# Performance work log

Measured on AMD Instinct MI355X. Metric: run time of the kernel, lower is better.

## Reference

```python
import math
import jax, jax.numpy as jnp
import numpy as np

B, NQ, NK, DIM, H, HD = 2, 1024, 2048, 1024, 16, 64


def setup_inputs() -> dict:
    key = jax.random.key(0)
    ks = jax.random.split(key, 12)
    s = 1.0 / math.sqrt(DIM)
    return {
        "q": jax.random.normal(ks[0], (B, NQ, DIM), jnp.float32),
        "k": jax.random.normal(ks[1], (B, NK, DIM), jnp.float32),
        "v": jax.random.normal(ks[2], (B, NK, DIM), jnp.float32),
        "distances": jax.random.uniform(ks[3], (B, NQ, NK), jnp.float32),
        "attn_mask": jax.random.bernoulli(ks[4], 0.5, (B, NQ, NK)),
        "key_padding_mask_q": jax.random.bernoulli(ks[5], 0.5, (B, NQ)),
        "key_padding_mask_k": jax.random.bernoulli(ks[6], 0.5, (B, NK)),
        "Wq": jax.random.normal(ks[7], (H * HD, DIM), jnp.float32) * s,
        "Wk": jax.random.normal(ks[8], (H * HD, DIM), jnp.float32) * s,
        "Wv": jax.random.normal(ks[9], (H * HD, DIM), jnp.float32) * s,
        "Wo": jax.random.normal(ks[10], (DIM, H * HD), jnp.float32) * s,
        "gate_alpha": jnp.float32(0.1),
    }


def reference(q, k, v, distances, attn_mask, key_padding_mask_q,
              key_padding_mask_k, Wq, Wk, Wv, Wo, gate_alpha):
    bsz, q_len, _ = q.shape
    k_len = k.shape[1]
    neg = jnp.finfo(q.dtype).min

    # projections -> (B, H, N, HD)
    qp = (q @ Wq.T).reshape(bsz, q_len, H, HD).transpose(0, 2, 1, 3)
    kp = (k @ Wk.T).reshape(bsz, k_len, H, HD).transpose(0, 2, 1, 3)
    vp = (v @ Wv.T).reshape(bsz, k_len, H, HD).transpose(0, 2, 1, 3)

    scores = jnp.einsum('bhqd,bhkd->bhqk', qp, kp) / math.sqrt(HD)
    scores = jnp.where(attn_mask[:, None, :, :], scores, neg)
    scores = jnp.where(key_padding_mask_k[:, None, None, :], scores, neg)

    attn = jax.nn.softmax(scores, axis=-1)  # (B,H,NQ,NK)

    # distance gating: mask, batch-mean normalize, exponential gate
    d = distances * attn_mask.astype(distances.dtype)
    d = d * key_padding_mask_k[:, None, :].astype(d.dtype)
    mean = d.sum(axis=(-1, -2)) / (q_len * k_len + 1e-6)
    mean = jnp.maximum(mean, 1e-6)[:, None, None]
    d = d / mean
    alpha = jax.nn.softplus(gate_alpha)
    gate = jnp.exp(-alpha * d)[:, None, :, :]  # (B,1,NQ,NK)

    w = attn * gate
    w = w / (w.sum(axis=-1, keepdims=True) + 1e-6)

    out = jnp.einsum('bhqk,bhkd->bhqd', w, vp)
    out = out.transpose(0, 2, 1, 3).reshape(bsz, q_len, H * HD)
    out = out * key_padding_mask_q[:, :, None].astype(out.dtype)
    return out @ Wo.T
```

## Files before the change

kernel.cpp:

```cpp
#include <hip/hip_runtime.h>
#include <hip/hip_bf16.h>
#include <cfloat>

#define B_   2
#define NQ_  1024
#define NK_  2048
#define H_   16
#define HD_  64
#define VPAD 2176
#define GPAD 2112

typedef float  floatx4 __attribute__((ext_vector_type(4)));
typedef __bf16 bf16x8  __attribute__((ext_vector_type(8)));
typedef __bf16 bf16x4  __attribute__((ext_vector_type(4)));

static __device__ __forceinline__ floatx4 mfma16(bf16x8 a, bf16x8 b, floatx4 c) {
    return __builtin_amdgcn_mfma_f32_16x16x32_bf16(a, b, c, 0, 0, 0);
}

static __device__ __forceinline__ void gl_lds(const __bf16* g, __bf16* lbase,
                                              int lane) {
#if __has_builtin(__builtin_amdgcn_global_load_lds)
    __builtin_amdgcn_global_load_lds(
        (const __attribute__((address_space(1))) void*)g,
        (__attribute__((address_space(3))) void*)lbase, 16, 0, 0);
#else
    *(bf16x8*)(lbase + lane * 8) = *(const bf16x8*)g;
#endif
}

struct CvtArgs {
    const float* src[7];
    __bf16*      dst[7];
};

__global__ __launch_bounds__(256) void cvt_mean_kernel(
    CvtArgs a, const float* __restrict__ dist, const int* __restrict__ amask,
    const int* __restrict__ kpmk, float* __restrict__ msum,
    __bf16* __restrict__ dmask)
{
    if (blockIdx.x >= 1792) {
        const int mb = blockIdx.x - 1792;
        const int b  = mb >> 9;
        const float* d  = dist  + (size_t)b * NQ_ * NK_;
        const int*   am = amask + (size_t)b * NQ_ * NK_;
        const int*   km = kpmk  + b * NK_;
        __bf16*      dm = dmask + (size_t)b * NQ_ * GPAD;
        const int base = (mb & 511) * 256 + threadIdx.x;
        float s = 0.f;
        #pragma unroll
        for (int j = 0; j < 4; j++) {
            const int i   = base + j * 131072;
            const int idx = i * 4;
            const int kk  = idx & (NK_ - 1);
            const int q   = i >> 9;
            float4 dv = *(const float4*)(d + idx);
            int4   mv = *(const int4*)(am + idx);
            int4   kv = *(const int4*)(km + kk);
            bf16x4 o;
            if (mv.x && kv.x) { s += dv.x; o[0] = (__bf16)dv.x; } else o[0] = (__bf16)3e38f;
            if (mv.y && kv.y) { s += dv.y; o[1] = (__bf16)dv.y; } else o[1] = (__bf16)3e38f;
            if (mv.z && kv.z) { s += dv.z; o[2] = (__bf16)dv.z; } else o[2] = (__bf16)3e38f;
            if (mv.w && kv.w) { s += dv.w; o[3] = (__bf16)dv.w; } else o[3] = (__bf16)3e38f;
            *(bf16x4*)&dm[(size_t)q * GPAD + kk] = o;
        }
        #pragma unroll
        for (int off = 32; off >= 1; off >>= 1) s += __shfl_down(s, off);
        __shared__ float wsum[4];
        if ((threadIdx.x & 63) == 0) wsum[threadIdx.x >> 6] = s;
        __syncthreads();
        if (threadIdx.x == 0)
            atomicAdd(&msum[b], wsum[0] + wsum[1] + wsum[2] + wsum[3]);
        return;
    }
    #pragma unroll
    for (int j = 0; j < 4; j++) {
        size_t r = (size_t)blockIdx.x * 1024 + j * 256 + threadIdx.x;
        int s;
        if (r < 262144)                  { s = 0; }
        else if ((r -= 262144) < 524288) { s = 1; }
        else if ((r -= 524288) < 524288) { s = 2; }
        else { r -= 524288; s = 3 + (int)(r >> 17); r &= 131071; }
        const float* sp = a.src[s] + r * 8;
        float4 f0 = *(const float4*)sp;
        float4 f1 = *(const float4*)(sp + 4);
        bf16x8 o;
        o[0] = (__bf16)f0.x; o[1] = (__bf16)f0.y; o[2] = (__bf16)f0.z; o[3] = (__bf16)f0.w;
        o[4] = (__bf16)f1.x; o[5] = (__bf16)f1.y; o[6] = (__bf16)f1.z; o[7] = (__bf16)f1.w;
        *(bf16x8*)(a.dst[s] + r * 8) = o;
    }
}

template <typename EPI>
static __device__ __forceinline__ void gemm128_core(
    const __bf16* __restrict__ A, const __bf16* __restrict__ Bw,
    int m0, int n0, __bf16* As, __bf16* Bs, EPI epi)
{
    const int t    = threadIdx.x;
    const int w    = t >> 6, lane = t & 63;
    const int lrow = lane & 15, quad = lane >> 4;
    const int lr   = lane >> 2, lc = lane & 3;

    floatx4 acc[4][4];
    #pragma unroll
    for (int mi = 0; mi < 4; mi++)
        #pragma unroll
        for (int ni = 0; ni < 4; ni++) acc[mi][ni] = floatx4{0.f, 0.f, 0.f, 0.f};

    const __bf16* ga = A  + (size_t)(m0 + w * 32 + lr) * 1024 + lc * 8;
    const __bf16* gb = Bw + (size_t)(n0 + w * 32 + lr) * 1024 + lc * 8;

    for (int k0 = 0; k0 < 1024; k0 += 64) {
        __syncthreads();
        #pragma unroll
        for (int h = 0; h < 2; h++) {
            gl_lds(ga + k0 + h * 32,             &As[h * 4096 + (w * 32) * 32],      lane);
            gl_lds(ga + k0 + h * 32 + 16 * 1024, &As[h * 4096 + (w * 32 + 16) * 32], lane);
            gl_lds(gb + k0 + h * 32,             &Bs[h * 4096 + (w * 32) * 32],      lane);
            gl_lds(gb + k0 + h * 32 + 16 * 1024, &Bs[h * 4096 + (w * 32 + 16) * 32], lane);
        }
        __syncthreads();

        #pragma unroll
        for (int h = 0; h < 2; h++) {
            bf16x8 af[4], bfr[4];
            #pragma unroll
            for (int mi = 0; mi < 4; mi++)
                af[mi] = *(const bf16x8*)
                    &As[h * 4096 + ((w & 1) * 64 + mi * 16 + lrow) * 32 + quad * 8];
            #pragma unroll
            for (int ni = 0; ni < 4; ni++)
                bfr[ni] = *(const bf16x8*)
                    &Bs[h * 4096 + ((w >> 1) * 64 + ni * 16 + lrow) * 32 + quad * 8];
            #pragma unroll
            for (int mi = 0; mi < 4; mi++)
                #pragma unroll
                for (int ni = 0; ni < 4; ni++)
                    acc[mi][ni] = mfma16(af[mi], bfr[ni], acc[mi][ni]);
        }
    }

    #pragma unroll
    for (int mi = 0; mi < 4; mi++)
        #pragma unroll
        for (int ni = 0; ni < 4; ni++)
            #pragma unroll
            for (int r = 0; r < 4; r++) {
                const int m = m0 + (w & 1) * 64 + mi * 16 + quad * 4 + r;
                const int n = n0 + (w >> 1) * 64 + ni * 16 + lrow;
                epi(m, n, acc[mi][ni][r]);
            }
}

template <typename EPI>
static __device__ __forceinline__ void gemm32_core(
    const __bf16* __restrict__ A, const __bf16* __restrict__ Bw,
    int m0, int n0, EPI epi)
{
    __shared__ alignas(16) __bf16 As[2][32 * 32];
    __shared__ alignas(16) __bf16 Bs[2][128 * 32];
    const int t    = threadIdx.x;
    const int w    = t >> 6, lane = t & 63;
    const int lrow = lane & 15, quad = lane >> 4;
    const int lr   = lane >> 2, lc = lane & 3;

    floatx4 acc[2][2];
    #pragma unroll
    for (int mi = 0; mi < 2; mi++)
        #pragma unroll
        for (int ni = 0; ni < 2; ni++) acc[mi][ni] = floatx4{0.f, 0.f, 0.f, 0.f};

    const __bf16* ga = A  + (size_t)(m0 + (w & 1) * 16 + lr) * 1024 + lc * 8;
    const __bf16* gb = Bw + (size_t)(n0 + w * 32 + lr) * 1024 + lc * 8;

    for (int k0 = 0; k0 < 1024; k0 += 64) {
        __syncthreads();
        #pragma unroll
        for (int h = 0; h < 2; h++) {
            if (w < 2)
                gl_lds(ga + k0 + h * 32, &As[h][(w * 16) * 32], lane);
            gl_lds(gb + k0 + h * 32,             &Bs[h][(w * 32) * 32],      lane);
            gl_lds(gb + k0 + h * 32 + 16 * 1024, &Bs[h][(w * 32 + 16) * 32], lane);
        }
        __syncthreads();

        #pragma unroll
        for (int h = 0; h < 2; h++) {
            bf16x8 af[2], bfr[2];
            #pragma unroll
            for (int mi = 0; mi < 2; mi++)
                af[mi] = *(const bf16x8*)
                    &As[h][(mi * 16 + lrow) * 32 + quad * 8];
            #pragma unroll
            for (int ni = 0; ni < 2; ni++)
                bfr[ni] = *(const bf16x8*)
                    &Bs[h][(w * 32 + ni * 16 + lrow) * 32 + quad * 8];
            #pragma unroll
            for (int mi = 0; mi < 2; mi++)
                #pragma unroll
                for (int ni = 0; ni < 2; ni++)
                    acc[mi][ni] = mfma16(af[mi], bfr[ni], acc[mi][ni]);
        }
    }

    #pragma unroll
    for (int mi = 0; mi < 2; mi++)
        #pragma unroll
        for (int ni = 0; ni < 2; ni++)
            #pragma unroll
            for (int r = 0; r < 4; r++) {
                const int m = m0 + mi * 16 + quad * 4 + r;
                const int n = n0 + w * 32 + ni * 16 + lrow;
                epi(m, n, acc[mi][ni][r]);
            }
}

__global__ __launch_bounds__(256) void proj_kernel(
    const __bf16* __restrict__ qb, const __bf16* __restrict__ kb,
    const __bf16* __restrict__ vb, const __bf16* __restrict__ wqb,
    const __bf16* __restrict__ wkb, const __bf16* __restrict__ wvb,
    __bf16* __restrict__ qp, __bf16* __restrict__ kp,
    __bf16* __restrict__ vpT)
{
    __shared__ alignas(16) __bf16 As[2 * 128 * 32];
    __shared__ alignas(16) __bf16 Bs[2 * 128 * 32];
    const int z = blockIdx.z;
    if (z == 0) {
        if ((int)blockIdx.x >= 16) return;
        gemm128_core(qb, wqb, blockIdx.x * 128, blockIdx.y * 128, As, Bs,
                     [&](int m, int n, float v) {
            const int b = m >> 10, q = m & 1023;
            const int h = n >> 6,  d = n & 63;
            qp[(((size_t)(b * 16 + h) * NQ_ + q) << 6) + d] = (__bf16)v;
        });
    } else if (z == 1) {
        gemm128_core(kb, wkb, blockIdx.x * 128, blockIdx.y * 128, As, Bs,
                     [&](int m, int n, float v) {
            const int b = m >> 11, key = m & 2047;
            const int h = n >> 6,  d = n & 63;
            kp[(((size_t)(b * 16 + h) * NK_ + key) << 6) + d] = (__bf16)v;
        });
    } else {
        gemm128_core(wvb, vb, blockIdx.y * 128, blockIdx.x * 128, As, Bs,
                     [&](int m, int n, float v) {
            const int h = m >> 6,  d = m & 63;
            const int b = n >> 11, key = n & 2047;
            vpT[((size_t)(b * 16 + h) * HD_ + d) * VPAD + key] = (__bf16)v;
        });
    }
}

__global__ __launch_bounds__(256) void oproj_kernel(
    const __bf16* __restrict__ A, const __bf16* __restrict__ W,
    float* __restrict__ Cout)
{
    const int m0 = blockIdx.x * 32, n0 = blockIdx.y * 128;
    gemm32_core(A, W, m0, n0, [&](int m, int n, float v) {
        Cout[(size_t)m * 1024 + n] = v;
    });
}

__global__ __launch_bounds__(256, 2) void attn_kernel(
    const __bf16* __restrict__ qp, const __bf16* __restrict__ kp,
    const __bf16* __restrict__ vpT, const __bf16* __restrict__ dmask,
    const float* __restrict__ msum, const float* __restrict__ galpha,
    float* __restrict__ Opart, float* __restrict__ Gpart)
{
    __shared__ __bf16 Ks[64 * 72];
    __shared__ __bf16 Vt[2][64 * 72];
    __shared__ __bf16 Ps[4][32 * 72];
    const int t    = threadIdx.x;
    const int w    = t >> 6, lane = t & 63;
    const int lrow = lane & 15, quad = lane >> 4;
    const int bid  = ((blockIdx.x & 7) << 6) | (blockIdx.x >> 3);
    const int qt   = bid & 7;
    const int bh   = (bid >> 3) & 31;
    const int z    = bid >> 8;
    const int b    = bh >> 4, h = bh & 15;
    const int q0   = qt * 128 + w * 32;
    const int kb0  = z * (NK_ / 2);
    const int NT   = NK_ / 128;

    const float mean  = fmaxf(msum[b] / ((float)(NQ_ * NK_) + 1e-6f), 1e-6f);
    const float alpha = log1pf(__expf(galpha[0]));
    const float cg    = -alpha / mean;

    bf16x8 qf0[2], qf1[2];
    #pragma unroll
    for (int g = 0; g < 2; g++) {
        const __bf16* qb = qp + ((size_t)bh * NQ_ + q0 + g * 16 + lrow) * HD_
                         + quad * 8;
        qf0[g] = *(const bf16x8*)qb;
        qf1[g] = *(const bf16x8*)(qb + 32);
    }

    const int srow0 = t >> 3,        sc0 = t & 7;
    const int srow1 = 32 + (t >> 3), sc1 = t & 7;
    const int so0 = srow0 * 72 + sc0 * 8;
    const int so1 = srow1 * 72 + sc1 * 8;
    const __bf16* Kg = kp  + ((size_t)bh * NK_ + kb0) * HD_;
    const __bf16* Vg = vpT + (size_t)bh * HD_ * VPAD + kb0;
    const __bf16* grow0 = dmask + ((size_t)b * NQ_ + q0 + lrow) * GPAD + kb0;
    const __bf16* grow1 = grow0 + (size_t)16 * GPAD;

    float G[2] = {0.f, 0.f};
    floatx4 O[2][4];
    #pragma unroll
    for (int g = 0; g < 2; g++)
        #pragma unroll
        for (int nb = 0; nb < 4; nb++) O[g][nb] = floatx4{0.f, 0.f, 0.f, 0.f};

    bf16x8 kr0, kr1, vr0, vr1;
    bf16x4 gr[2][4];
    auto loadt = [&](int kb) {
        kr0 = *(const bf16x8*)(Kg + (size_t)(kb + srow0) * HD_ + sc0 * 8);
        kr1 = *(const bf16x8*)(Kg + (size_t)(kb + srow1) * HD_ + sc1 * 8);
        vr0 = *(const bf16x8*)(Vg + (size_t)srow0 * VPAD + kb + sc0 * 8);
        vr1 = *(const bf16x8*)(Vg + (size_t)srow1 * VPAD + kb + sc1 * 8);
        #pragma unroll
        for (int c = 0; c < 4; c++) {
            gr[0][c] = *(const bf16x4*)(grow0 + kb + c * 16 + quad * 4);
            gr[1][c] = *(const bf16x4*)(grow1 + kb + c * 16 + quad * 4);
        }
    };
    loadt(0);

    for (int ib = 0; ib < NT; ib++) {
        const int kb  = ib * 64;
        const int cur = ib & 1;

        __syncthreads();
        *(bf16x8*)&Ks[so0]      = kr0;
        *(bf16x8*)&Ks[so1]      = kr1;
        *(bf16x8*)&Vt[cur][so0] = vr0;
        *(bf16x8*)&Vt[cur][so1] = vr1;
        __syncthreads();

        bf16x4 gcur[2][4];
        #pragma unroll
        for (int g = 0; g < 2; g++)
            #pragma unroll
            for (int c = 0; c < 4; c++) gcur[g][c] = gr[g][c];
        if (ib + 1 < NT) loadt(kb + 64);

        __builtin_amdgcn_s_setprio(1);
        floatx4 s4[2][4];
        #pragma unroll
        for (int c = 0; c < 4; c++) {
            bf16x8 kf0 = *(const bf16x8*)&Ks[(c * 16 + lrow) * 72 + quad * 8];
            bf16x8 kf1 = *(const bf16x8*)&Ks[(c * 16 + lrow) * 72 + 32 + quad * 8];
            #pragma unroll
            for (int g = 0; g < 2; g++) {
                floatx4 a = floatx4{0.f, 0.f, 0.f, 0.f};
                a = mfma16(kf0, qf0[g], a);
                a = mfma16(kf1, qf1[g], a);
                s4[g][c] = a;
            }
        }

        if (ib > 0) {
            const int prv = cur ^ 1;
            bf16x8 pf0[2], pf1[2];
            #pragma unroll
            for (int g = 0; g < 2; g++) {
                pf0[g] = *(const bf16x8*)&Ps[w][(g * 16 + lrow) * 72 + quad * 8];
                pf1[g] = *(const bf16x8*)&Ps[w][(g * 16 + lrow) * 72 + 32 + quad * 8];
            }
            #pragma unroll
            for (int nb = 0; nb < 4; nb++) {
                bf16x8 vf0 = *(const bf16x8*)
                    &Vt[prv][(nb * 16 + lrow) * 72 + quad * 8];
                bf16x8 vf1 = *(const bf16x8*)
                    &Vt[prv][(nb * 16 + lrow) * 72 + 32 + quad * 8];
                #pragma unroll
                for (int g = 0; g < 2; g++) {
                    O[g][nb] = mfma16(pf0[g], vf0, O[g][nb]);
                    O[g][nb] = mfma16(pf1[g], vf1, O[g][nb]);
                }
            }
        }
        __builtin_amdgcn_s_setprio(0);

        #pragma unroll
        for (int g = 0; g < 2; g++)
            #pragma unroll
            for (int c = 0; c < 4; c++) {
                const float e0 = __expf(fmaf(s4[g][c][0], 0.125f, cg * (float)gcur[g][c][0]));
                const float e1 = __expf(fmaf(s4[g][c][1], 0.125f, cg * (float)gcur[g][c][1]));
                const float e2 = __expf(fmaf(s4[g][c][2], 0.125f, cg * (float)gcur[g][c][2]));
                const float e3 = __expf(fmaf(s4[g][c][3], 0.125f, cg * (float)gcur[g][c][3]));
                G[g] += (e0 + e1) + (e2 + e3);
                bf16x4 pk;
                pk[0] = (__bf16)e0; pk[1] = (__bf16)e1;
                pk[2] = (__bf16)e2; pk[3] = (__bf16)e3;
                *(bf16x4*)&Ps[w][(g * 16 + lrow) * 72 + c * 16 + quad * 4] = pk;
            }
    }

    {
        const int prv = (NT - 1) & 1;
        bf16x8 pf0[2], pf1[2];
        #pragma unroll
        for (int g = 0; g < 2; g++) {
            pf0[g] = *(const bf16x8*)&Ps[w][(g * 16 + lrow) * 72 + quad * 8];
            pf1[g] = *(const bf16x8*)&Ps[w][(g * 16 + lrow) * 72 + 32 + quad * 8];
        }
        #pragma unroll
        for (int nb = 0; nb < 4; nb++) {
            bf16x8 vf0 = *(const bf16x8*)&Vt[prv][(nb * 16 + lrow) * 72 + quad * 8];
            bf16x8 vf1 = *(const bf16x8*)&Vt[prv][(nb * 16 + lrow) * 72 + 32 + quad * 8];
            #pragma unroll
            for (int g = 0; g < 2; g++) {
                O[g][nb] = mfma16(pf0[g], vf0, O[g][nb]);
                O[g][nb] = mfma16(pf1[g], vf1, O[g][nb]);
            }
        }
    }

    #pragma unroll
    for (int g = 0; g < 2; g++) {
        G[g] += __shfl_xor(G[g], 16);
        G[g] += __shfl_xor(G[g], 32);
    }

    #pragma unroll
    for (int g = 0; g < 2; g++) {
        float* Op = Opart + (size_t)z * (B_ * NQ_ * 1024)
                          + ((size_t)b * NQ_ + q0 + g * 16) * 1024 + h * HD_;
        #pragma unroll
        for (int r = 0; r < 4; r++) {
            const int qr = quad * 4 + r;
            #pragma unroll
            for (int nb = 0; nb < 4; nb++)
                Op[(size_t)qr * 1024 + nb * 16 + lrow] = O[g][nb][r];
        }
        if (lane < 16)
            Gpart[(size_t)z * (32 * 1024) + bh * 1024 + q0 + g * 16 + lane] = G[g];
    }
}

__global__ __launch_bounds__(256) void combine_kernel(
    const float* __restrict__ Opart, const float* __restrict__ Gpart,
    const int* __restrict__ kpmq, __bf16* __restrict__ attnout)
{
    const int idx = blockIdx.x * 256 + threadIdx.x;
    const int m   = idx >> 8;
    const int c4  = (idx & 255) * 4;
    const int b   = m >> 10, q = m & 1023;
    const int h   = c4 >> 6;
    const float g = Gpart[(b * 16 + h) * 1024 + q]
                  + Gpart[32 * 1024 + (b * 16 + h) * 1024 + q];
    const float f = kpmq[b * NQ_ + q] ? 1.f / (g + 1e-30f) : 0.f;
    const float4 o0 = *(const float4*)(Opart + (size_t)m * 1024 + c4);
    const float4 o1 = *(const float4*)(Opart + (size_t)(B_ * NQ_) * 1024
                                              + (size_t)m * 1024 + c4);
    bf16x4 r;
    r[0] = (__bf16)((o0.x + o1.x) * f);
    r[1] = (__bf16)((o0.y + o1.y) * f);
    r[2] = (__bf16)((o0.z + o1.z) * f);
    r[3] = (__bf16)((o0.w + o1.w) * f);
    *(bf16x4*)&attnout[(size_t)m * 1024 + c4] = r;
}

extern "C" void kernel_launch(void* const* d_in, const int* in_sizes, int n_in,
                              void* d_out, int out_size, void* d_ws,
                              size_t ws_size, hipStream_t stream)
{
    const float* q      = (const float*)d_in[0];
    const float* k      = (const float*)d_in[1];
    const float* v      = (const float*)d_in[2];
    const float* dist   = (const float*)d_in[3];
    const int*   amask  = (const int*)d_in[4];
    const int*   kpmq   = (const int*)d_in[5];
    const int*   kpmk   = (const int*)d_in[6];
    const float* Wq     = (const float*)d_in[7];
    const float* Wk     = (const float*)d_in[8];
    const float* Wv     = (const float*)d_in[9];
    const float* Wo     = (const float*)d_in[10];
    const float* galpha = (const float*)d_in[11];

    char* p = (char*)d_ws;
    float*  msum = (float*)p;                 p += 256;
    __bf16* qb   = (__bf16*)p;                p += (size_t)2097152 * 2;
    __bf16* kb   = (__bf16*)p;                p += (size_t)4194304 * 2;
    __bf16* vb   = (__bf16*)p;                p += (size_t)4194304 * 2;
    __bf16* wqb  = (__bf16*)p;                p += (size_t)1048576 * 2;
    __bf16* wkb  = (__bf16*)p;                p += (size_t)1048576 * 2;
    __bf16* wvb  = (__bf16*)p;                p += (size_t)1048576 * 2;
    __bf16* wob  = (__bf16*)p;                p += (size_t)1048576 * 2;
    __bf16* qp   = (__bf16*)p;                p += (size_t)2097152 * 2;
    __bf16* kpb  = (__bf16*)p;                p += (size_t)4194304 * 2;
    __bf16* vpT  = (__bf16*)p;                p += (size_t)32 * 64 * VPAD * 2;
    __bf16* dmask = (__bf16*)p;               p += (size_t)2048 * GPAD * 2;
    __bf16* attnout = (__bf16*)p;             p += (size_t)2097152 * 2;

    float* Opart = (float*)kb;
    float* Gpart = (float*)qb;

    CvtArgs ca;
    ca.src[0] = q;  ca.src[1] = k;  ca.src[2] = v;
    ca.src[3] = Wq; ca.src[4] = Wk; ca.src[5] = Wv; ca.src[6] = Wo;
    ca.dst[0] = qb;  ca.dst[1] = kb;  ca.dst[2] = vb;
    ca.dst[3] = wqb; ca.dst[4] = wkb; ca.dst[5] = wvb; ca.dst[6] = wob;

    hipMemsetAsync(msum, 0, 256, stream);
    cvt_mean_kernel<<<2816, 256, 0, stream>>>(ca, dist, amask, kpmk, msum,
                                              dmask);
    proj_kernel<<<dim3(32, 8, 3), 256, 0, stream>>>(qb, kb, vb, wqb, wkb, wvb,
                                                    qp, kpb, vpT);
    attn_kernel<<<512, 256, 0, stream>>>(qp, kpb, vpT, dmask,
                                         msum, galpha, Opart, Gpart);
    combine_kernel<<<2048, 256, 0, stream>>>(Opart, Gpart, kpmq, attnout);
    oproj_kernel<<<dim3(64, 8), 256, 0, stream>>>(attnout, wob, (float*)d_out);
}
```

Measured before the change: 245.9 us.

## Load K/V fragments directly from global into registers, dropping LDS staging and barriers

The attention kernel stops staging K and V tiles through shared memory. Each wave now loads its own MFMA fragments straight from global memory into registers, with K prefetched one tile ahead and V loaded after use, so the two __syncthreads per tile disappear. The exponential also switches to exp2f with pre-scaled constants. The cost is that each of the four waves fetches the same K/V data separately (more global/L2 traffic), register pressure rises, and V loads are exposed with less prefetch distance.

```diff
diff --git a/kernel.cpp b/kernel.cpp
--- a/kernel.cpp
+++ b/kernel.cpp
@@ -266,8 +266,6 @@
     const float* __restrict__ msum, const float* __restrict__ galpha,
     float* __restrict__ Opart, float* __restrict__ Gpart)
 {
-    __shared__ __bf16 Ks[64 * 72];
-    __shared__ __bf16 Vt[2][64 * 72];
     __shared__ __bf16 Ps[4][32 * 72];
     const int t    = threadIdx.x;
     const int w    = t >> 6, lane = t & 63;
@@ -284,6 +282,8 @@
     const float mean  = fmaxf(msum[b] / ((float)(NQ_ * NK_) + 1e-6f), 1e-6f);
     const float alpha = log1pf(__expf(galpha[0]));
     const float cg    = -alpha / mean;
+    const float cg2   = cg * 1.44269504f;
+    const float s2    = 0.125f * 1.44269504f;
 
     bf16x8 qf0[2], qf1[2];
     #pragma unroll
@@ -294,10 +294,6 @@
         qf1[g] = *(const bf16x8*)(qb + 32);
     }
 
-    const int srow0 = t >> 3,        sc0 = t & 7;
-    const int srow1 = 32 + (t >> 3), sc1 = t & 7;
-    const int so0 = srow0 * 72 + sc0 * 8;
-    const int so1 = srow1 * 72 + sc1 * 8;
     const __bf16* Kg = kp  + ((size_t)bh * NK_ + kb0) * HD_;
     const __bf16* Vg = vpT + (size_t)bh * HD_ * VPAD + kb0;
     const __bf16* grow0 = dmask + ((size_t)b * NQ_ + q0 + lrow) * GPAD + kb0;
@@ -310,56 +306,58 @@
         #pragma unroll
         for (int nb = 0; nb < 4; nb++) O[g][nb] = floatx4{0.f, 0.f, 0.f, 0.f};
 
-    bf16x8 kr0, kr1, vr0, vr1;
-    bf16x4 gr[2][4];
-    auto loadt = [&](int kb) {
-        kr0 = *(const bf16x8*)(Kg + (size_t)(kb + srow0) * HD_ + sc0 * 8);
-        kr1 = *(const bf16x8*)(Kg + (size_t)(kb + srow1) * HD_ + sc1 * 8);
-        vr0 = *(const bf16x8*)(Vg + (size_t)srow0 * VPAD + kb + sc0 * 8);
-        vr1 = *(const bf16x8*)(Vg + (size_t)srow1 * VPAD + kb + sc1 * 8);
+    bf16x8 kf0[4], kf1[4];
+    bf16x8 vf0[4], vf1[4];
+    bf16x4 grc[2][4];
+
+    auto loadK = [&](int kb) {
         #pragma unroll
         for (int c = 0; c < 4; c++) {
-            gr[0][c] = *(const bf16x4*)(grow0 + kb + c * 16 + quad * 4);
-            gr[1][c] = *(const bf16x4*)(grow1 + kb + c * 16 + quad * 4);
+            const __bf16* kr = Kg + (size_t)(kb + c * 16 + lrow) * HD_ + quad * 8;
+            kf0[c] = *(const bf16x8*)kr;
+            kf1[c] = *(const bf16x8*)(kr + 32);
         }
     };
-    loadt(0);
+    auto loadV = [&](int kb) {
+        #pragma unroll
+        for (int nb = 0; nb < 4; nb++) {
+            const __bf16* vr = Vg + (size_t)(nb * 16 + lrow) * VPAD + kb + quad * 8;
+            vf0[nb] = *(const bf16x8*)vr;
+            vf1[nb] = *(const bf16x8*)(vr + 32);
+        }
+    };
+    auto loadG = [&](int kb) {
+        #pragma unroll
+        for (int c = 0; c < 4; c++) {
+            grc[0][c] = *(const bf16x4*)(grow0 + kb + c * 16 + quad * 4);
+            grc[1][c] = *(const bf16x4*)(grow1 + kb + c * 16 + quad * 4);
+        }
+    };
+
+    loadK(0);
+    loadG(0);
 
     for (int ib = 0; ib < NT; ib++) {
-        const int kb  = ib * 64;
-        const int cur = ib & 1;
-
-        __syncthreads();
-        *(bf16x8*)&Ks[so0]      = kr0;
-        *(bf16x8*)&Ks[so1]      = kr1;
-        *(bf16x8*)&Vt[cur][so0] = vr0;
-        *(bf16x8*)&Vt[cur][so1] = vr1;
-        __syncthreads();
-
-        bf16x4 gcur[2][4];
-        #pragma unroll
-        for (int g = 0; g < 2; g++)
-            #pragma unroll
-            for (int c = 0; c < 4; c++) gcur[g][c] = gr[g][c];
-        if (ib + 1 < NT) loadt(kb + 64);
+        const int kb = ib * 64;
 
         __builtin_amdgcn_s_setprio(1);
         floatx4 s4[2][4];
         #pragma unroll
         for (int c = 0; c < 4; c++) {
-            bf16x8 kf0 = *(const bf16x8*)&Ks[(c * 16 + lrow) * 72 + quad * 8];
-            bf16x8 kf1 = *(const bf16x8*)&Ks[(c * 16 + lrow) * 72 + 32 + quad * 8];
             #pragma unroll
             for (int g = 0; g < 2; g++) {
                 floatx4 a = floatx4{0.f, 0.f, 0.f, 0.f};
-                a = mfma16(kf0, qf0[g], a);
-                a = mfma16(kf1, qf1[g], a);
+                a = mfma16(kf0[c], qf0[g], a);
+                a = mfma16(kf1[c], qf1[g], a);
                 s4[g][c] = a;
             }
         }
+        __builtin_amdgcn_s_setprio(0);
+
+        if (ib + 1 < NT) loadK(kb + 64);
 
         if (ib > 0) {
-            const int prv = cur ^ 1;
+            __builtin_amdgcn_s_setprio(1);
             bf16x8 pf0[2], pf1[2];
             #pragma unroll
             for (int g = 0; g < 2; g++) {
@@ -368,37 +366,36 @@
             }
             #pragma unroll
             for (int nb = 0; nb < 4; nb++) {
-                bf16x8 vf0 = *(const bf16x8*)
-                    &Vt[prv][(nb * 16 + lrow) * 72 + quad * 8];
-                bf16x8 vf1 = *(const bf16x8*)
-                    &Vt[prv][(nb * 16 + lrow) * 72 + 32 + quad * 8];
                 #pragma unroll
                 for (int g = 0; g < 2; g++) {
-                    O[g][nb] = mfma16(pf0[g], vf0, O[g][nb]);
-                    O[g][nb] = mfma16(pf1[g], vf1, O[g][nb]);
+                    O[g][nb] = mfma16(pf0[g], vf0[nb], O[g][nb]);
+                    O[g][nb] = mfma16(pf1[g], vf1[nb], O[g][nb]);
                 }
             }
-        }
-        __builtin_amdgcn_s_setprio(0);
+            __builtin_amdgcn_s_setprio(0);
+        }
+
+        loadV(kb);
 
         #pragma unroll
         for (int g = 0; g < 2; g++)
             #pragma unroll
             for (int c = 0; c < 4; c++) {
-                const float e0 = __expf(fmaf(s4[g][c][0], 0.125f, cg * (float)gcur[g][c][0]));
-                const float e1 = __expf(fmaf(s4[g][c][1], 0.125f, cg * (float)gcur[g][c][1]));
-                const float e2 = __expf(fmaf(s4[g][c][2], 0.125f, cg * (float)gcur[g][c][2]));
-                const float e3 = __expf(fmaf(s4[g][c][3], 0.125f, cg * (float)gcur[g][c][3]));
+                const float e0 = exp2f(fmaf(s4[g][c][0], s2, cg2 * (float)grc[g][c][0]));
+                const float e1 = exp2f(fmaf(s4[g][c][1], s2, cg2 * (float)grc[g][c][1]));
+                const float e2 = exp2f(fmaf(s4[g][c][2], s2, cg2 * (float)grc[g][c][2]));
+                const float e3 = exp2f(fmaf(s4[g][c][3], s2, cg2 * (float)grc[g][c][3]));
                 G[g] += (e0 + e1) + (e2 + e3);
                 bf16x4 pk;
                 pk[0] = (__bf16)e0; pk[1] = (__bf16)e1;
                 pk[2] = (__bf16)e2; pk[3] = (__bf16)e3;
                 *(bf16x4*)&Ps[w][(g * 16 + lrow) * 72 + c * 16 + quad * 4] = pk;
             }
+
+        if (ib + 1 < NT) loadG(kb + 64);
     }
 
     {
-        const int prv = (NT - 1) & 1;
         bf16x8 pf0[2], pf1[2];
         #pragma unroll
         for (int g = 0; g < 2; g++) {
@@ -407,12 +404,10 @@
         }
         #pragma unroll
         for (int nb = 0; nb < 4; nb++) {
-            bf16x8 vf0 = *(const bf16x8*)&Vt[prv][(nb * 16 + lrow) * 72 + quad * 8];
-            bf16x8 vf1 = *(const bf16x8*)&Vt[prv][(nb * 16 + lrow) * 72 + 32 + quad * 8];
             #pragma unroll
             for (int g = 0; g < 2; g++) {
-                O[g][nb] = mfma16(pf0[g], vf0, O[g][nb]);
-                O[g][nb] = mfma16(pf1[g], vf1, O[g][nb]);
+                O[g][nb] = mfma16(pf0[g], vf0[nb], O[g][nb]);
+                O[g][nb] = mfma16(pf1[g], vf1[nb], O[g][nb]);
             }
         }
     }
```

Result: slower. 295.6 us (+20.2%).
